# Kernel tuning notes

Measured on AMD Instinct MI355X. Metric: run time of the kernel, lower is better.

The kernel has to match this reference:

```python
import jax, jax.numpy as jnp
import numpy as np

IMAGE_SIZE = 224
COV_HP = 1.0
SIGMA = 1.0
STEPS = 2
CUTOFF = 20.0
IMP_LO, IMP_HI = 0.5, 2.0
REL_W = 0.5
EPS = 1e-6

# Projection matrices for front/top/left views (buffer Js in the module)
JS = jnp.array([[[1, 0, 0], [0, 1, 0]],
                [[1, 0, 0], [0, 0, 1]],
                [[0, 0, 1], [0, 1, 0]]], dtype=jnp.float32)


def _blur(d, sigma):
    # d: [B,H,W]; separable Gaussian blur, 'same' padding
    r = max(1, int(3 * sigma))
    x = jnp.arange(-r, r + 1, dtype=jnp.float32)
    k = jnp.exp(-(x * x) / (2.0 * sigma * sigma))
    k = k / k.sum()
    d4 = d[:, None]  # [B,1,H,W]
    kh = k.reshape(1, 1, -1, 1)
    kw = k.reshape(1, 1, 1, -1)
    d4 = jax.lax.conv_general_dilated(d4, kh, (1, 1), [(r, r), (0, 0)],
                                      dimension_numbers=('NCHW', 'OIHW', 'NCHW'))
    d4 = jax.lax.conv_general_dilated(d4, kw, (1, 1), [(0, 0), (r, r)],
                                      dimension_numbers=('NCHW', 'OIHW', 'NCHW'))
    return d4[:, 0]


def _fill_depth_map(d, sigma, steps):
    # fill_depth_map is not defined in the source; implemented as iterative
    # Gaussian-blur hole filling (empty pixels take blurred neighborhood).
    for _ in range(steps):
        b = _blur(d, sigma)
        d = jnp.where(d > 1e-6, d, b)
    return d


def _forward(position, cov3d, opacity, importance):
    B, N, _ = position.shape
    H = W = IMAGE_SIZE
    Hh, Wh = H // 2, W // 2
    yy, xx = jnp.meshgrid(jnp.arange(Hh), jnp.arange(Wh), indexing='ij')
    grid = jnp.stack([xx, yy], axis=-1).astype(jnp.float32)  # [Hh,Wh,2]
    imp = jnp.clip(jnp.broadcast_to(importance[:, :N], (B, N)), IMP_LO, IMP_HI)
    imp = imp[:, :, None, None]
    eye3 = jnp.eye(3, dtype=cov3d.dtype)
    eye2 = jnp.eye(2, dtype=cov3d.dtype)
    maps = []
    for v in range(3):  # fixed small view loop, as in the source
        J = JS[v]  # [2,3]
        # NOTE: source mutates cov3d across the view loop; replicate that
        cov3d = (cov3d + jnp.swapaxes(cov3d, -1, -2)) * 0.5
        cov3d = cov3d + EPS * eye3
        nrm = jnp.linalg.norm(cov3d, axis=(-1, -2), keepdims=True)
        cov3d = cov3d / (nrm + EPS) * COV_HP
        cinv = jnp.linalg.inv(cov3d)                               # [B,N,3,3]
        cov2d_inv = jnp.einsum('ij,bnjk,lk->bnil', J, cinv, J)     # J C^-1 J^T
        cov2d_inv = cov2d_inv + eye2 * (EPS * 1e-4)
        proj = jnp.einsum('bnk,jk->bnj', position, J)              # [B,N,2]
        mn = proj.min(axis=1, keepdims=True)
        mx = proj.max(axis=1, keepdims=True)
        rng = mx - mn + 1e-6
        mn = mn - 0.5 * rng
        mx = mx + 0.5 * rng
        rng = mx - mn + 1e-6
        xy = jnp.clip((proj - mn) / rng * (Wh - 1), 0.0, Wh - 1)
        delta = grid[None, None] - xy[:, :, None, None, :]         # [B,N,Hh,Wh,2]
        mask_h = jnp.linalg.norm(delta, axis=-1) < CUTOFF
        mask = jnp.repeat(jnp.repeat(mask_h, 2, axis=2), 2, axis=3)
        exph = -jnp.einsum('bnhwj,bnjk,bnhwk->bnhw', delta, cov2d_inv, delta)
        exp_full = jax.image.resize(exph, (B, N, H, W), method='bilinear')
        exp_full = jnp.clip(exp_full, -20.0, 0.0)
        w = opacity[:, :, None, None] * imp * jnp.exp(exp_full)
        w = jnp.where(mask, w, 0.0)
        wmin = w.min(axis=1, keepdims=True)
        wmax = w.max(axis=1, keepdims=True)
        nw = (w - wmin) / (wmax - wmin + EPS) * REL_W + w / (w.sum(axis=1, keepdims=True) + EPS)
        dm = nw.sum(axis=1)  # [B,H,W]
        maps.append(_fill_depth_map(dm, SIGMA, STEPS))
    d = jnp.stack(maps, axis=1)  # [B,3,H,W], already 224x224 so resize is a no-op
    d = (d - d.mean()) / (jnp.std(d, ddof=1) + EPS)
    return d


def setup_inputs() -> dict:
    key = jax.random.key(0)
    k1, k2, k3 = jax.random.split(key, 3)
    B, N, MAXG = 1, 512, 1000
    return {
        'position': jax.random.normal(k1, (B, N, 3), dtype=jnp.float32),
        'cov3d': jax.random.normal(k2, (B, N, 3, 3), dtype=jnp.float32),
        'opacity': jax.random.uniform(k3, (B, N), dtype=jnp.float32),
        'importance': jnp.ones((1, MAXG), dtype=jnp.float32),
    }


def reference(position, cov3d, opacity, importance):
    return _forward(position, cov3d, opacity, importance)
```

## Files before the change

kernel.cpp:

```cpp
#include <hip/hip_runtime.h>
#include <math.h>


#define NBLOCKS 588u
#define NARR 32
#define FLAG_IDX (NARR * 32)
#define KSPLIT 4

__device__ __forceinline__ float g_ld(const float* p) {
    return __hip_atomic_load(p, __ATOMIC_RELAXED, __HIP_MEMORY_SCOPE_AGENT);
}
__device__ __forceinline__ void g_st(float* p, float v) {
    __hip_atomic_store(p, v, __ATOMIC_RELAXED, __HIP_MEMORY_SCOPE_AGENT);
}

__device__ __forceinline__ void grid_barrier(unsigned* cnts, int arrIdx, bool poller) {
    __syncthreads();
    if (threadIdx.x == 0) {
        asm volatile("s_waitcnt vmcnt(0)" ::: "memory");
        __hip_atomic_fetch_add(&cnts[arrIdx * 32], 1u,
                               __ATOMIC_RELAXED, __HIP_MEMORY_SCOPE_AGENT);
        unsigned* flagp = &cnts[FLAG_IDX];
        if (poller) {
            for (;;) {
                unsigned s = 0;
                #pragma unroll
                for (int i = 0; i < NARR; ++i)
                    s += __hip_atomic_load(&cnts[i * 32],
                                           __ATOMIC_RELAXED, __HIP_MEMORY_SCOPE_AGENT);
                if (s == NBLOCKS) break;
                __builtin_amdgcn_s_sleep(2);
            }
            asm volatile("" ::: "memory");
            __hip_atomic_store(flagp, 1u, __ATOMIC_RELAXED, __HIP_MEMORY_SCOPE_AGENT);
        } else {
            while (__hip_atomic_load(flagp, __ATOMIC_RELAXED,
                                     __HIP_MEMORY_SCOPE_AGENT) == 0u)
                __builtin_amdgcn_s_sleep(2);
        }
    }
    __syncthreads();
}

__device__ __forceinline__ float wave_min(float v) {
    #pragma unroll
    for (int o = 32; o >= 1; o >>= 1) v = fminf(v, __shfl_xor(v, o));
    return v;
}

__global__ __launch_bounds__(512) void splat_part_kernel(
    const float* __restrict__ position, const float* __restrict__ cov3d,
    const float* __restrict__ opacity, const float* __restrict__ importance,
    float* __restrict__ part, unsigned* __restrict__ cnts) {
    __shared__ float4 lsA[512];
    __shared__ float2 lsB[512];
    __shared__ float red[8 * 6];
    __shared__ int wcnt[8];
    __shared__ float4 pS[7][64], pMn[7][64], pMx[7][64];
    const int v  = blockIdx.z >> 2;
    const int kk = blockIdx.z & 3;
    const int tx0 = blockIdx.x * 16, ty0 = blockIdx.y * 16;
    const int tid = threadIdx.x;
    const int lane = tid & 63, wave = tid >> 6;

    if (blockIdx.x == 0 && blockIdx.y == 0 && blockIdx.z == 0) {
        for (int i = tid; i <= FLAG_IDX; i += 512) cnts[i] = 0;
    }

    const int n = tid;
    const float p0 = position[n * 3 + 0];
    const float p1 = position[n * 3 + 1];
    const float p2 = position[n * 3 + 2];
    const float opimp = opacity[n] * fminf(fmaxf(importance[n], 0.5f), 2.0f);

    {
        float vals[6] = {p0, -p0, p1, -p1, p2, -p2};
        #pragma unroll
        for (int q = 0; q < 6; ++q) {
            float r = wave_min(vals[q]);
            if (lane == 0) red[wave * 6 + q] = r;
        }
    }
    __syncthreads();
    float mn6[6];
    #pragma unroll
    for (int q = 0; q < 6; ++q) {
        float r = red[q];
        #pragma unroll
        for (int w = 1; w < 8; ++w) r = fminf(r, red[w * 6 + q]);
        mn6[q] = r;
    }
    const float pmn[3] = {mn6[0], mn6[2], mn6[4]};
    const float pmx[3] = {-mn6[1], -mn6[3], -mn6[5]};

    float c00 = cov3d[n * 9 + 0], c01 = cov3d[n * 9 + 1], c02 = cov3d[n * 9 + 2];
    float c10 = cov3d[n * 9 + 3], c11 = cov3d[n * 9 + 4], c12 = cov3d[n * 9 + 5];
    float c20 = cov3d[n * 9 + 6], c21 = cov3d[n * 9 + 7], c22 = cov3d[n * 9 + 8];
    for (int vv = 0; vv <= v; ++vv) {
        float s01 = 0.5f * (c01 + c10);
        float s02 = 0.5f * (c02 + c20);
        float s12 = 0.5f * (c12 + c21);
        float s00 = c00 + 1e-6f;
        float s11 = c11 + 1e-6f;
        float s22 = c22 + 1e-6f;
        float nrm = sqrtf(s00 * s00 + s11 * s11 + s22 * s22 +
                          2.0f * (s01 * s01 + s02 * s02 + s12 * s12));
        float inv = 1.0f / (nrm + 1e-6f);
        c00 = s00 * inv; c11 = s11 * inv; c22 = s22 * inv;
        c01 = s01 * inv; c10 = c01; c02 = s02 * inv; c20 = c02;
        c12 = s12 * inv; c21 = c12;
    }
    float cof00 = c11 * c22 - c12 * c12;
    float cof01 = c02 * c12 - c01 * c22;
    float cof02 = c01 * c12 - c02 * c11;
    float det = c00 * cof00 + c01 * cof01 + c02 * cof02;
    float idet = 1.0f / det;
    float i00 = cof00 * idet;
    float i01 = cof01 * idet;
    float i02 = cof02 * idet;
    float i11 = (c00 * c22 - c02 * c02) * idet;
    float i12 = (c02 * c01 - c00 * c12) * idet;
    float i22 = (c00 * c11 - c01 * c01) * idet;

    float Aa, Ab, Ac, prx, pry;
    int ix, iy;
    if (v == 0)      { Aa = i00; Ab = i01; Ac = i11; prx = p0; pry = p1; ix = 0; iy = 1; }
    else if (v == 1) { Aa = i00; Ab = i02; Ac = i22; prx = p0; pry = p2; ix = 0; iy = 2; }
    else             { Aa = i22; Ab = i12; Ac = i11; prx = p2; pry = p1; ix = 2; iy = 1; }
    Aa += 1e-10f;
    Ac += 1e-10f;

    float mnx = pmn[ix], mxx = pmx[ix], mny = pmn[iy], mxy = pmx[iy];
    float rngx = mxx - mnx + 1e-6f;
    float mnx2 = mnx - 0.5f * rngx;
    float mxx2 = mxx + 0.5f * rngx;
    rngx = mxx2 - mnx2 + 1e-6f;
    float rngy = mxy - mny + 1e-6f;
    float mny2 = mny - 0.5f * rngy;
    float mxy2 = mxy + 0.5f * rngy;
    rngy = mxy2 - mny2 + 1e-6f;
    float gx = fminf(fmaxf((prx - mnx2) / rngx * 111.0f, 0.0f), 111.0f);
    float gy = fminf(fmaxf((pry - mny2) / rngy * 111.0f, 0.0f), 111.0f);

    unsigned long long m;
    bool pass;
    {
        const float bx0 = (float)(tx0 >> 1), bx1 = (float)((tx0 + 15) >> 1);
        const float by0 = (float)(ty0 >> 1), by1 = (float)((ty0 + 15) >> 1);
        float dx = fmaxf(fmaxf(bx0 - gx, gx - bx1), 0.0f);
        float dy = fmaxf(fmaxf(by0 - gy, gy - by1), 0.0f);
        pass = (dx * dx + dy * dy) < 400.01f;
        m = __ballot(pass);
        if (lane == 0) wcnt[wave] = __popcll(m);
    }
    __syncthreads();
    int base = 0, lentot = 0;
    #pragma unroll
    for (int w = 0; w < 8; ++w) {
        int c = wcnt[w];
        if (w < wave) base += c;
        lentot += c;
    }
    if (pass) {
        int slot = base + __popcll(m & ((1ull << lane) - 1ull));
        lsA[slot] = make_float4(Aa, 2.0f * Ab, Ac, opimp);
        lsB[slot] = make_float2(gx, gy);
    }
    __syncthreads();
    const int len = lentot;

    const int qx = lane & 7, qy = lane >> 3;
    const int xh = (tx0 >> 1) + qx;
    const int yh = (ty0 >> 1) + qy;

    const int npad = (len + 63) & ~63;
    if (tid < npad - len) {
        lsA[len + tid] = make_float4(1.0f, 0.0f, 1.0f, 0.0f);
        lsB[len + tid] = make_float2(1e9f, 1e9f);
    }
    __syncthreads();

    float exA[2], eyA[2], VxA[2], VyA[2];
    #pragma unroll
    for (int p = 0; p < 2; ++p) {
        int xlo = xh - 1 + p; int xhi = min(xlo + 1, 111); xlo = max(xlo, 0);
        float wlo = p ? 0.75f : 0.25f, whi = 1.0f - wlo;
        exA[p] = wlo * (float)xlo + whi * (float)xhi;
        VxA[p] = wlo * whi * (float)(xhi - xlo) * (float)(xhi - xlo);
        int ylo = yh - 1 + p; int yhi2 = min(ylo + 1, 111); ylo = max(ylo, 0);
        eyA[p] = wlo * (float)ylo + whi * (float)yhi2;
        VyA[p] = wlo * whi * (float)(yhi2 - ylo) * (float)(yhi2 - ylo);
    }
    const float fxh = (float)xh, fyh = (float)yh;

    const int chunk = npad >> 5;
    const int cbeg = ((kk << 3) + wave) * chunk, cend = cbeg + chunk;

    float S00 = 0.f, S01 = 0.f, S10 = 0.f, S11 = 0.f;
    float mn00 = INFINITY, mn01 = INFINITY, mn10 = INFINITY, mn11 = INFINITY;
    float mx00 = -INFINITY, mx01 = -INFINITY, mx10 = -INFINITY, mx11 = -INFINITY;

    for (int i = cbeg; i < cend; i += 2) {
        float4 gA0 = lsA[i], gA1 = lsA[i + 1];
        float2 gB0 = lsB[i], gB1 = lsB[i + 1];
        #pragma unroll
        for (int u = 0; u < 2; ++u) {
            const float4 gA = u ? gA1 : gA0;
            const float2 gB = u ? gB1 : gB0;
            const float a = gA.x, b2 = gA.y, c = gA.z, op = gA.w;
            const float xx = gB.x, yy = gB.y;
            const float dxh = fxh - xx, dyh = fyh - yy;
            const bool inside = dxh * dxh + dyh * dyh < 400.0f;
            const float dx0 = exA[0] - xx, dx1 = exA[1] - xx;
            const float dy0 = eyA[0] - yy, dy1 = eyA[1] - yy;
            const float adx0 = a * dx0, adx1 = a * dx1;
            const float bdy0 = b2 * dy0, bdy1 = b2 * dy1;
            const float cdy0 = c * dy0 * dy0, cdy1 = c * dy1 * dy1;
            const float ax0 = a * VxA[0], ax1 = a * VxA[1];
            const float cy0 = c * VyA[0], cy1 = c * VyA[1];
            #pragma unroll
            for (int py = 0; py < 2; ++py) {
                const float bdyp = py ? bdy1 : bdy0;
                const float cdyp = py ? cdy1 : cdy0;
                const float cyp  = py ? cy1 : cy0;
                #pragma unroll
                for (int px = 0; px < 2; ++px) {
                    const float dxp  = px ? dx1 : dx0;
                    const float adxp = px ? adx1 : adx0;
                    const float axp  = px ? ax1 : ax0;
                    float q = dxp * (adxp + bdyp) + cdyp;
                    float bil = -((q + axp) + cyp);
                    bil = fminf(fmaxf(bil, -20.0f), 0.0f);
                    bil = inside ? bil : -1e9f;
                    float w = op * __expf(bil);
                    if (py == 0 && px == 0) { S00 += w; mn00 = fminf(mn00, w); mx00 = fmaxf(mx00, w); }
                    if (py == 0 && px == 1) { S01 += w; mn01 = fminf(mn01, w); mx01 = fmaxf(mx01, w); }
                    if (py == 1 && px == 0) { S10 += w; mn10 = fminf(mn10, w); mx10 = fmaxf(mx10, w); }
                    if (py == 1 && px == 1) { S11 += w; mn11 = fminf(mn11, w); mx11 = fmaxf(mx11, w); }
                }
            }
        }
    }
    if (wave > 0) {
        pS[wave - 1][lane]  = make_float4(S00, S01, S10, S11);
        pMn[wave - 1][lane] = make_float4(mn00, mn01, mn10, mn11);
        pMx[wave - 1][lane] = make_float4(mx00, mx01, mx10, mx11);
    }
    __syncthreads();
    if (wave == 0) {
        #pragma unroll
        for (int w = 0; w < 7; ++w) {
            float4 s = pS[w][lane], mnw = pMn[w][lane], mxw = pMx[w][lane];
            S00 += s.x; S01 += s.y; S10 += s.z; S11 += s.w;
            mn00 = fminf(mn00, mnw.x); mn01 = fminf(mn01, mnw.y);
            mn10 = fminf(mn10, mnw.z); mn11 = fminf(mn11, mnw.w);
            mx00 = fmaxf(mx00, mxw.x); mx01 = fmaxf(mx01, mxw.y);
            mx10 = fmaxf(mx10, mxw.z); mx11 = fmaxf(mx11, mxw.w);
        }
        if (len < 512) {
            mn00 = fminf(mn00, 0.f); mn01 = fminf(mn01, 0.f);
            mn10 = fminf(mn10, 0.f); mn11 = fminf(mn11, 0.f);
            mx00 = fmaxf(mx00, 0.f); mx01 = fmaxf(mx01, 0.f);
            mx10 = fmaxf(mx10, 0.f); mx11 = fmaxf(mx11, 0.f);
        }
        float S4[4]  = {S00, S01, S10, S11};
        float mn4[4] = {mn00, mn01, mn10, mn11};
        float mx4[4] = {mx00, mx01, mx10, mx11};
        #pragma unroll
        for (int pp = 0; pp < 4; ++pp) {
            const int py = pp >> 1, px = pp & 1;
            const int y = ty0 + 2 * qy + py, x = tx0 + 2 * qx + px;
            float* pb = part + ((v * 224 + y) * 224 + x) * 12 + kk;
            pb[0] = S4[pp];
            pb[4] = mn4[pp];
            pb[8] = mx4[pp];
        }
    }
}

__global__ __launch_bounds__(256, 3) void blur_norm_kernel(
    const float* __restrict__ part, float* __restrict__ out,
    float2* __restrict__ partials, unsigned* __restrict__ cnts) {
    __shared__ float A[28 * 29];
    __shared__ float T[28 * 29];
    __shared__ float r1[4], r2[4];
    __shared__ double s1[256], s2[256];
    const int v = blockIdx.z;
    const int tx0 = blockIdx.x * 16, ty0 = blockIdx.y * 16;
    const int tid = threadIdx.x;
    const int lane = tid & 63, wave = tid >> 6;
    const int bid = (v * 14 + blockIdx.y) * 14 + blockIdx.x;
    const float kw[7] = {0.00443305f, 0.05400558f, 0.24203623f, 0.39905030f,
                         0.24203623f, 0.05400558f, 0.00443305f};

    for (int idx = tid; idx < 28 * 28; idx += 256) {
        int rr = idx / 28, c = idx % 28;
        int gyy = ty0 - 6 + rr, gxx = tx0 - 6 + c;
        float val = 0.0f;
        if (gyy >= 0 && gyy < 224 && gxx >= 0 && gxx < 224) {
            const float* pb = part + ((v * 224 + gyy) * 224 + gxx) * 12;
            const float4 Sv  = *(const float4*)(pb);
            const float4 mnv = *(const float4*)(pb + 4);
            const float4 mxv = *(const float4*)(pb + 8);
            float S  = (Sv.x + Sv.y) + (Sv.z + Sv.w);
            float mn = fminf(fminf(mnv.x, mnv.y), fminf(mnv.z, mnv.w));
            float mx = fmaxf(fmaxf(mxv.x, mxv.y), fmaxf(mxv.z, mxv.w));
            val = 0.5f * (S - 512.0f * mn) / (mx - mn + 1e-6f) + S / (S + 1e-6f);
        }
        A[rr * 29 + c] = val;
    }
    __syncthreads();
    for (int idx = tid; idx < 22 * 28; idx += 256) {
        int rr = 3 + idx / 28, c = idx % 28;
        float s = 0.0f;
        #pragma unroll
        for (int i = 0; i < 7; ++i) s += kw[i] * A[(rr - 3 + i) * 29 + c];
        T[rr * 29 + c] = s;
    }
    __syncthreads();
    for (int idx = tid; idx < 22 * 22; idx += 256) {
        int rr = 3 + idx / 22, c = 3 + idx % 22;
        int gyy = ty0 - 6 + rr, gxx = tx0 - 6 + c;
        float s = 0.0f;
        #pragma unroll
        for (int j = 0; j < 7; ++j) s += kw[j] * T[rr * 29 + c - 3 + j];
        float ctr = A[rr * 29 + c];
        float d1 = ctr > 1e-6f ? ctr : s;
        if (gyy < 0 || gyy > 223 || gxx < 0 || gxx > 223) d1 = 0.0f;
        A[rr * 29 + c] = d1;
    }
    __syncthreads();
    for (int idx = tid; idx < 16 * 22; idx += 256) {
        int rr = 6 + idx / 22, c = 3 + idx % 22;
        float s = 0.0f;
        #pragma unroll
        for (int i = 0; i < 7; ++i) s += kw[i] * A[(rr - 3 + i) * 29 + c];
        T[rr * 29 + c] = s;
    }
    __syncthreads();
    const int rr2 = 6 + (tid >> 4), cc2 = 6 + (tid & 15);
    float d2;
    {
        float s = 0.0f;
        #pragma unroll
        for (int j = 0; j < 7; ++j) s += kw[j] * T[rr2 * 29 + cc2 - 3 + j];
        float ctr = A[rr2 * 29 + cc2];
        d2 = ctr > 1e-6f ? ctr : s;
    }
    float ls1 = d2, ls2 = d2 * d2;
    #pragma unroll
    for (int o = 32; o >= 1; o >>= 1) {
        ls1 += __shfl_xor(ls1, o);
        ls2 += __shfl_xor(ls2, o);
    }
    if (lane == 0) { r1[wave] = ls1; r2[wave] = ls2; }
    __syncthreads();
    if (tid == 0) {
        float a = r1[0] + r1[1] + r1[2] + r1[3];
        float b = r2[0] + r2[1] + r2[2] + r2[3];
        float* pb = (float*)&partials[bid];
        g_st(pb + 0, a);
        g_st(pb + 1, b);
    }

    grid_barrier(cnts, bid & (NARR - 1), bid == 0);

    double a = 0.0, b = 0.0;
    const float* pb = (const float*)partials;
    for (int i = tid; i < 588; i += 256) {
        a += (double)g_ld(pb + 2 * i);
        b += (double)g_ld(pb + 2 * i + 1);
    }
    s1[tid] = a; s2[tid] = b;
    __syncthreads();
    for (int s = 128; s >= 1; s >>= 1) {
        if (tid < s) { s1[tid] += s1[tid + s]; s2[tid] += s2[tid + s]; }
        __syncthreads();
    }
    const double M = 150528.0;
    double mean = s1[0] / M;
    double var = (s2[0] - M * mean * mean) / (M - 1.0);
    double sd = sqrt(var > 0.0 ? var : 0.0);
    const float fmean = (float)mean;
    const float finv = 1.0f / ((float)sd + 1e-6f);
    out[(v * 224 + ty0 + (tid >> 4)) * 224 + tx0 + (tid & 15)] =
        (d2 - fmean) * finv;
}

extern "C" void kernel_launch(void* const* d_in, const int* in_sizes, int n_in,
                              void* d_out, int out_size, void* d_ws, size_t ws_size,
                              hipStream_t stream) {
    const float* position   = (const float*)d_in[0];
    const float* cov3d      = (const float*)d_in[1];
    const float* opacity    = (const float*)d_in[2];
    const float* importance = (const float*)d_in[3];
    float* out = (float*)d_out;

    float* part      = (float*)d_ws;
    float2* partials = (float2*)((float*)d_ws + 1806336);
    unsigned* cnts   = (unsigned*)((float*)d_ws + 1806336 + 1176);

    hipLaunchKernelGGL(splat_part_kernel, dim3(14, 14, 3 * KSPLIT), dim3(512), 0,
                       stream, position, cov3d, opacity, importance, part, cnts);
    hipLaunchKernelGGL(blur_norm_kernel, dim3(14, 14, 3), dim3(256), 0, stream,
                       part, out, partials, cnts);
}
```

Baseline: 108.8 us.

## Hoist per-gaussian setup into separate kernel and store partials as float4 planes

Moves the per-gaussian covariance inversion, bounds reduction and projection into a small 3-block setup kernel that writes packed conic/opacity and screen coordinates. Every splat block previously recomputed these, so the splat blocks now only load them. The partial sums, mins and maxes are also stored as three separate float4 planes, one float4 per 2x2 quad, in place of a strided 12-float interleave. This gives coalesced vector stores, while the blur kernel now does four scalar gathers per component. It also adds a kernel launch and a dependency on the setup kernel finishing first.

```diff
diff --git a/kernel.cpp b/kernel.cpp
--- a/kernel.cpp
+++ b/kernel.cpp
@@ -6,6 +6,9 @@
 #define NARR 32
 #define FLAG_IDX (NARR * 32)
 #define KSPLIT 4
+#define QOFF 12544
+#define MNOFF 602112
+#define MXOFF 1204224
 
 __device__ __forceinline__ float g_ld(const float* p) {
     return __hip_atomic_load(p, __ATOMIC_RELAXED, __HIP_MEMORY_SCOPE_AGENT);
@@ -48,22 +51,17 @@
     return v;
 }
 
-__global__ __launch_bounds__(512) void splat_part_kernel(
+__global__ __launch_bounds__(512) void setup_kernel(
     const float* __restrict__ position, const float* __restrict__ cov3d,
     const float* __restrict__ opacity, const float* __restrict__ importance,
-    float* __restrict__ part, unsigned* __restrict__ cnts) {
-    __shared__ float4 lsA[512];
-    __shared__ float2 lsB[512];
+    float4* __restrict__ abc, float2* __restrict__ gxy,
+    unsigned* __restrict__ cnts) {
     __shared__ float red[8 * 6];
-    __shared__ int wcnt[8];
-    __shared__ float4 pS[7][64], pMn[7][64], pMx[7][64];
-    const int v  = blockIdx.z >> 2;
-    const int kk = blockIdx.z & 3;
-    const int tx0 = blockIdx.x * 16, ty0 = blockIdx.y * 16;
+    const int v = blockIdx.x;
     const int tid = threadIdx.x;
     const int lane = tid & 63, wave = tid >> 6;
 
-    if (blockIdx.x == 0 && blockIdx.y == 0 && blockIdx.z == 0) {
+    if (v == 0) {
         for (int i = tid; i <= FLAG_IDX; i += 512) cnts[i] = 0;
     }
 
@@ -76,19 +74,19 @@
     {
         float vals[6] = {p0, -p0, p1, -p1, p2, -p2};
         #pragma unroll
-        for (int q = 0; q < 6; ++q) {
-            float r = wave_min(vals[q]);
-            if (lane == 0) red[wave * 6 + q] = r;
+        for (int k = 0; k < 6; ++k) {
+            float r = wave_min(vals[k]);
+            if (lane == 0) red[wave * 6 + k] = r;
         }
     }
     __syncthreads();
     float mn6[6];
     #pragma unroll
-    for (int q = 0; q < 6; ++q) {
-        float r = red[q];
-        #pragma unroll
-        for (int w = 1; w < 8; ++w) r = fminf(r, red[w * 6 + q]);
-        mn6[q] = r;
+    for (int k = 0; k < 6; ++k) {
+        float r = red[k];
+        #pragma unroll
+        for (int w = 1; w < 8; ++w) r = fminf(r, red[w * 6 + k]);
+        mn6[k] = r;
     }
     const float pmn[3] = {mn6[0], mn6[2], mn6[4]};
     const float pmx[3] = {-mn6[1], -mn6[3], -mn6[5]};
@@ -142,13 +140,33 @@
     float gx = fminf(fmaxf((prx - mnx2) / rngx * 111.0f, 0.0f), 111.0f);
     float gy = fminf(fmaxf((pry - mny2) / rngy * 111.0f, 0.0f), 111.0f);
 
+    abc[v * 512 + n] = make_float4(Aa, 2.0f * Ab, Ac, opimp);
+    gxy[v * 512 + n] = make_float2(gx, gy);
+}
+
+__global__ __launch_bounds__(512) void splat_part_kernel(
+    const float4* __restrict__ abc, const float2* __restrict__ gxy,
+    float* __restrict__ part) {
+    __shared__ float4 lsA[512];
+    __shared__ float2 lsB[512];
+    __shared__ int wcnt[8];
+    __shared__ float4 pS[7][64], pMn[7][64], pMx[7][64];
+    const int v  = blockIdx.z >> 2;
+    const int kk = blockIdx.z & 3;
+    const int tx0 = blockIdx.x * 16, ty0 = blockIdx.y * 16;
+    const int tid = threadIdx.x;
+    const int lane = tid & 63, wave = tid >> 6;
+
+    const float4 a4 = abc[v * 512 + tid];
+    const float2 g2 = gxy[v * 512 + tid];
+
     unsigned long long m;
     bool pass;
     {
         const float bx0 = (float)(tx0 >> 1), bx1 = (float)((tx0 + 15) >> 1);
         const float by0 = (float)(ty0 >> 1), by1 = (float)((ty0 + 15) >> 1);
-        float dx = fmaxf(fmaxf(bx0 - gx, gx - bx1), 0.0f);
-        float dy = fmaxf(fmaxf(by0 - gy, gy - by1), 0.0f);
+        float dx = fmaxf(fmaxf(bx0 - g2.x, g2.x - bx1), 0.0f);
+        float dy = fmaxf(fmaxf(by0 - g2.y, g2.y - by1), 0.0f);
         pass = (dx * dx + dy * dy) < 400.01f;
         m = __ballot(pass);
         if (lane == 0) wcnt[wave] = __popcll(m);
@@ -163,8 +181,8 @@
     }
     if (pass) {
         int slot = base + __popcll(m & ((1ull << lane) - 1ull));
-        lsA[slot] = make_float4(Aa, 2.0f * Ab, Ac, opimp);
-        lsB[slot] = make_float2(gx, gy);
+        lsA[slot] = a4;
+        lsB[slot] = g2;
     }
     __syncthreads();
     const int len = lentot;
@@ -263,18 +281,10 @@
             mx00 = fmaxf(mx00, 0.f); mx01 = fmaxf(mx01, 0.f);
             mx10 = fmaxf(mx10, 0.f); mx11 = fmaxf(mx11, 0.f);
         }
-        float S4[4]  = {S00, S01, S10, S11};
-        float mn4[4] = {mn00, mn01, mn10, mn11};
-        float mx4[4] = {mx00, mx01, mx10, mx11};
-        #pragma unroll
-        for (int pp = 0; pp < 4; ++pp) {
-            const int py = pp >> 1, px = pp & 1;
-            const int y = ty0 + 2 * qy + py, x = tx0 + 2 * qx + px;
-            float* pb = part + ((v * 224 + y) * 224 + x) * 12 + kk;
-            pb[0] = S4[pp];
-            pb[4] = mn4[pp];
-            pb[8] = mx4[pp];
-        }
+        const int qidx = (kk * 3 + v) * QOFF + yh * 112 + xh;
+        ((float4*)(part))[qidx]          = make_float4(S00, S01, S10, S11);
+        ((float4*)(part + MNOFF))[qidx]  = make_float4(mn00, mn01, mn10, mn11);
+        ((float4*)(part + MXOFF))[qidx]  = make_float4(mx00, mx01, mx10, mx11);
     }
 }
 
@@ -298,13 +308,16 @@
         int gyy = ty0 - 6 + rr, gxx = tx0 - 6 + c;
         float val = 0.0f;
         if (gyy >= 0 && gyy < 224 && gxx >= 0 && gxx < 224) {
-            const float* pb = part + ((v * 224 + gyy) * 224 + gxx) * 12;
-            const float4 Sv  = *(const float4*)(pb);
-            const float4 mnv = *(const float4*)(pb + 4);
-            const float4 mxv = *(const float4*)(pb + 8);
-            float S  = (Sv.x + Sv.y) + (Sv.z + Sv.w);
-            float mn = fminf(fminf(mnv.x, mnv.y), fminf(mnv.z, mnv.w));
-            float mx = fmaxf(fmaxf(mxv.x, mxv.y), fmaxf(mxv.z, mxv.w));
+            const int qb = (gyy >> 1) * 112 + (gxx >> 1);
+            const int comp = ((gyy & 1) << 1) | (gxx & 1);
+            float S = 0.0f, mn = INFINITY, mx = -INFINITY;
+            #pragma unroll
+            for (int k = 0; k < KSPLIT; ++k) {
+                const int fi = ((k * 3 + v) * QOFF + qb) * 4 + comp;
+                S += part[fi];
+                mn = fminf(mn, part[MNOFF + fi]);
+                mx = fmaxf(mx, part[MXOFF + fi]);
+            }
             val = 0.5f * (S - 512.0f * mn) / (mx - mn + 1e-6f) + S / (S + 1e-6f);
         }
         A[rr * 29 + c] = val;
@@ -399,9 +412,13 @@
     float* part      = (float*)d_ws;
     float2* partials = (float2*)((float*)d_ws + 1806336);
     unsigned* cnts   = (unsigned*)((float*)d_ws + 1806336 + 1176);
-
+    float4* abc      = (float4*)((float*)d_ws + 1808640);
+    float2* gxy      = (float2*)((float*)d_ws + 1808640 + 6144);
+
+    hipLaunchKernelGGL(setup_kernel, dim3(3), dim3(512), 0, stream,
+                       position, cov3d, opacity, importance, abc, gxy, cnts);
     hipLaunchKernelGGL(splat_part_kernel, dim3(14, 14, 3 * KSPLIT), dim3(512), 0,
-                       stream, position, cov3d, opacity, importance, part, cnts);
+                       stream, abc, gxy, part);
     hipLaunchKernelGGL(blur_norm_kernel, dim3(14, 14, 3), dim3(256), 0, stream,
                        part, out, partials, cnts);
 }
```

New measurement: 97.02 us. 10.8% less time.
